# Kernel tuning notes

Hardware: AMD Instinct MI355X
Metric: run time of the kernel (lower is better)

## Reference

```python
import jax, jax.numpy as jnp
import numpy as np

N_NODES = 50000
N_EDGES = 400000
D_PROT = 512
D_TEXT = 2048
GN_EPS = 1e-5


def setup_inputs() -> dict:
    key = jax.random.key(0)
    ks = jax.random.split(key, 8)
    s = 0.02
    return {
        "x": jax.random.normal(ks[0], (N_NODES, D_PROT), jnp.float32),
        "edge_index": jax.random.randint(ks[1], (2, N_EDGES), 0, N_NODES, dtype=jnp.int32),
        "gn_weight": jnp.ones((D_PROT,), jnp.float32),
        "gn_bias": jnp.zeros((D_PROT,), jnp.float32),
        "gn_mean_scale": jnp.ones((D_PROT,), jnp.float32),
        "conv1_w": jax.random.normal(ks[2], (D_PROT, D_PROT), jnp.float32) * s,
        "conv1_b": jnp.zeros((D_PROT,), jnp.float32),
        "conv2_w": jax.random.normal(ks[3], (D_PROT, D_PROT), jnp.float32) * s,
        "conv2_b": jnp.zeros((D_PROT,), jnp.float32),
        "proj1_w": jax.random.normal(ks[4], (D_TEXT, D_PROT), jnp.float32) * s,
        "proj1_b": jnp.zeros((D_TEXT,), jnp.float32),
        "proj2_w": jax.random.normal(ks[5], (D_TEXT, D_TEXT), jnp.float32) * s,
        "proj2_b": jnp.zeros((D_TEXT,), jnp.float32),
    }


def _graph_norm(x, weight, bias, mean_scale):
    # PyG GraphNorm over a single graph: shift by mean_scale*mean, scale by rstd
    mean = jnp.mean(x, axis=0, keepdims=True)            # [1, D]
    out = x - mean * mean_scale
    var = jnp.mean(out * out, axis=0, keepdims=True)     # [1, D]
    out = out * jax.lax.rsqrt(var + GN_EPS)
    return out * weight + bias


def _sgconv(x, src, dst, w, b):
    # SGConv K=1 with GCN normalization and added self-loops:
    n = x.shape[0]
    deg = jax.ops.segment_sum(jnp.ones_like(src, dtype=x.dtype), dst, num_segments=n) + 1.0
    dinv = jax.lax.rsqrt(deg)                            # [N]
    norm = dinv[src] * dinv[dst]                         # [E]
    agg = jax.ops.segment_sum(x[src] * norm[:, None], dst, num_segments=n)
    agg = agg + x * (dinv * dinv)[:, None]               # self-loop contribution
    return agg @ w.T + b


def reference(x, edge_index, gn_weight, gn_bias, gn_mean_scale,
              conv1_w, conv1_b, conv2_w, conv2_b,
              proj1_w, proj1_b, proj2_w, proj2_b):
    src, dst = edge_index[0], edge_index[1]
    h = _graph_norm(x, gn_weight, gn_bias, gn_mean_scale)
    h = jax.nn.relu(_sgconv(h, src, dst, conv1_w, conv1_b))  # dropout = identity (eval)
    h = jax.nn.relu(_sgconv(h, src, dst, conv2_w, conv2_b))
    h = h @ proj1_w.T + proj1_b
    h = jax.nn.gelu(h, approximate=False)
    h = h @ proj2_w.T + proj2_b
    return h
```

## Files before the change

### kernel.cpp

```cpp
#include <hip/hip_runtime.h>
#include <math.h>

typedef _Float16 half_t;
typedef _Float16 f16x2 __attribute__((ext_vector_type(2)));
typedef _Float16 f16x4 __attribute__((ext_vector_type(4)));
typedef _Float16 f16x8 __attribute__((ext_vector_type(8)));
typedef float f32x4 __attribute__((ext_vector_type(4)));

#define D_PROT 512
#define D_TEXT 2048

__global__ void k_cvt4(const float* __restrict__ s, half_t* __restrict__ d, int n4) {
    int i = blockIdx.x * 256 + threadIdx.x;
    if (i < n4) {
        float4 v = ((const float4*)s)[i];
        f16x4 o;
        o.x = (_Float16)v.x; o.y = (_Float16)v.y;
        o.z = (_Float16)v.z; o.w = (_Float16)v.w;
        ((f16x4*)d)[i] = o;
    }
}

__global__ void k_deg(const int* __restrict__ dst, int E, int* __restrict__ deg) {
    int i = blockIdx.x * 256 + threadIdx.x;
    if (i < E) atomicAdd(&deg[dst[i]], 1);
}

__global__ void k_dinv(const int* __restrict__ deg, float* __restrict__ dinv, int n) {
    int i = blockIdx.x * 256 + threadIdx.x;
    if (i < n) dinv[i] = rsqrtf((float)deg[i] + 1.0f);
}

__global__ void k_blocksum(const int* __restrict__ deg, int* __restrict__ bsum, int n) {
    __shared__ int sd[256];
    int i = blockIdx.x * 256 + threadIdx.x;
    sd[threadIdx.x] = (i < n) ? deg[i] : 0;
    __syncthreads();
    for (int s = 128; s > 0; s >>= 1) {
        if (threadIdx.x < s) sd[threadIdx.x] += sd[threadIdx.x + s];
        __syncthreads();
    }
    if (threadIdx.x == 0) bsum[blockIdx.x] = sd[0];
}

__global__ void k_scan_bsum(const int* __restrict__ bsum, int* __restrict__ boff, int nb) {
    if (threadIdx.x == 0 && blockIdx.x == 0) {
        int acc = 0;
        for (int i = 0; i < nb; i++) { boff[i] = acc; acc += bsum[i]; }
    }
}

__global__ void k_scan_final(const int* __restrict__ deg, const int* __restrict__ boff,
                             int* __restrict__ rowptr, int n) {
    __shared__ int sd[256];
    int i = blockIdx.x * 256 + threadIdx.x;
    int v = (i < n) ? deg[i] : 0;
    sd[threadIdx.x] = v;
    __syncthreads();
    for (int s = 1; s < 256; s <<= 1) {
        int t2 = (threadIdx.x >= s) ? sd[threadIdx.x - s] : 0;
        __syncthreads();
        sd[threadIdx.x] += t2;
        __syncthreads();
    }
    if (i < n) rowptr[i + 1] = boff[blockIdx.x] + sd[threadIdx.x];
}

__global__ void k_fill(const int* __restrict__ src, const int* __restrict__ dst, int E,
                       const int* __restrict__ rowptr, int* __restrict__ fill,
                       int* __restrict__ colidx) {
    int i = blockIdx.x * 256 + threadIdx.x;
    if (i < E) {
        int d = dst[i];
        int pos = atomicAdd(&fill[d], 1);
        colidx[rowptr[d] + pos] = src[i];
    }
}

__global__ void k_gnreduce(const float* __restrict__ x, float* __restrict__ sums,
                           float* __restrict__ sumsq, int Nn) {
    int t = threadIdx.x;
    int c = t * 2;
    float s0 = 0, s1 = 0, q0 = 0, q1 = 0;
    for (int r = blockIdx.x; r < Nn; r += gridDim.x) {
        float2 v = *(const float2*)(x + (size_t)r * D_PROT + c);
        s0 += v.x; s1 += v.y; q0 += v.x * v.x; q1 += v.y * v.y;
    }
    atomicAdd(&sums[c], s0);  atomicAdd(&sums[c + 1], s1);
    atomicAdd(&sumsq[c], q0); atomicAdd(&sumsq[c + 1], q1);
}

__global__ void k_gnfinal(const float* __restrict__ sums, const float* __restrict__ sumsq,
                          const float* __restrict__ w, const float* __restrict__ b,
                          const float* __restrict__ ms, float* __restrict__ ab, float invN) {
    int d = blockIdx.x * 256 + threadIdx.x;
    if (d < D_PROT) {
        float mean = sums[d] * invN;
        float m2 = sumsq[d] * invN;
        float mm = mean * ms[d];
        float var = m2 - 2.f * mm * mean + mm * mm;
        float rstd = rsqrtf(var + 1e-5f);
        float a = rstd * w[d];
        ab[d] = a;
        ab[D_PROT + d] = b[d] - mm * a;
    }
}

__global__ void k_gnnorm(const float* __restrict__ x, const float* __restrict__ ab,
                         half_t* __restrict__ h, int n4) {
    int i = blockIdx.x * 256 + threadIdx.x;
    if (i < n4) {
        size_t idx = (size_t)i * 4;
        float4 v = *(const float4*)(x + idx);
        int d = (int)(idx & (D_PROT - 1));
        const float* a = ab;
        const float* bb = ab + D_PROT;
        f16x4 o;
        o.x = (_Float16)(v.x * a[d]     + bb[d]);
        o.y = (_Float16)(v.y * a[d + 1] + bb[d + 1]);
        o.z = (_Float16)(v.z * a[d + 2] + bb[d + 2]);
        o.w = (_Float16)(v.w * a[d + 3] + bb[d + 3]);
        *(f16x4*)(h + idx) = o;
    }
}

__global__ void k_agg(const half_t* __restrict__ h, half_t* __restrict__ out,
                      const int* __restrict__ rowptr, const int* __restrict__ colidx,
                      const float* __restrict__ dinv) {
    int node = blockIdx.x;
    int t = threadIdx.x;
    float di = dinv[node];
    int beg = rowptr[node], end = rowptr[node + 1];
    const f16x4* hp = (const f16x4*)h;
    f16x4 sv = hp[node * 128 + t];
    float dii = di * di;
    float a0 = (float)sv.x * dii, a1 = (float)sv.y * dii;
    float a2 = (float)sv.z * dii, a3 = (float)sv.w * dii;
    int e = beg;
    for (; e + 4 <= end; e += 4) {
        int s0 = colidx[e],     s1 = colidx[e + 1];
        int s2 = colidx[e + 2], s3 = colidx[e + 3];
        float w0 = dinv[s0] * di, w1 = dinv[s1] * di;
        float w2 = dinv[s2] * di, w3 = dinv[s3] * di;
        f16x4 v0 = hp[s0 * 128 + t], v1 = hp[s1 * 128 + t];
        f16x4 v2 = hp[s2 * 128 + t], v3 = hp[s3 * 128 + t];
        a0 += w0 * (float)v0.x + w1 * (float)v1.x + w2 * (float)v2.x + w3 * (float)v3.x;
        a1 += w0 * (float)v0.y + w1 * (float)v1.y + w2 * (float)v2.y + w3 * (float)v3.y;
        a2 += w0 * (float)v0.z + w1 * (float)v1.z + w2 * (float)v2.z + w3 * (float)v3.z;
        a3 += w0 * (float)v0.w + w1 * (float)v1.w + w2 * (float)v2.w + w3 * (float)v3.w;
    }
    for (; e < end; ++e) {
        int s = colidx[e];
        float wgt = dinv[s] * di;
        f16x4 v = hp[s * 128 + t];
        a0 += wgt * (float)v.x; a1 += wgt * (float)v.y;
        a2 += wgt * (float)v.z; a3 += wgt * (float)v.w;
    }
    f16x4 o;
    o.x = (_Float16)a0; o.y = (_Float16)a1; o.z = (_Float16)a2; o.w = (_Float16)a3;
    ((f16x4*)out)[node * 128 + t] = o;
}

#define FENCE() asm volatile("" ::: "memory")
#define BAR()   do { FENCE(); __builtin_amdgcn_s_barrier(); FENCE(); } while (0)
#define WAITV4() asm volatile("s_waitcnt vmcnt(4)" ::: "memory")
#define WAITV0() asm volatile("s_waitcnt vmcnt(0)" ::: "memory")
#define GLD(src, dst) __builtin_amdgcn_global_load_lds( \
    (const __attribute__((address_space(1))) void*)(src), \
    (__attribute__((address_space(3))) void*)(dst), 16, 0, 0)
#define LDF(base, row, kk) \
    (*(const f16x8*)((base) + ((((row) * 128 + (kk) * 64 + fqo)) ^ (((row) & 7) << 4))))
#define MM(mi, nj, A_, B_) \
    acc[mi][nj] = __builtin_amdgcn_mfma_f32_16x16x32_f16(A_, B_, acc[mi][nj], 0, 0, 0)

template <int ACT, typename OUT_T>
__global__ __launch_bounds__(512, 2) void k_gemm8(const half_t* __restrict__ A,
                                                  const half_t* __restrict__ W,
                                                  const float* __restrict__ bias,
                                                  OUT_T* __restrict__ C,
                                                  int M, int N, int K) {
    __shared__ half_t sm[2][32768];
    const int bn = blockIdx.x * 256;
    const int bm = blockIdx.y * 256;

    const int t = threadIdx.x;
    const int w = t >> 6, lane = t & 63;
    const int fr = lane & 15, fq = lane >> 4;
    const int fqo = fq * 16;
    const int wm = (w >> 2) * 128, wn = (w & 3) * 64;
    const int NT = K >> 6;

    int q0 = w * 512 + lane * 8;
    int q1 = 4096 + q0;
    int s0 = q0 ^ (((q0 >> 6) & 7) << 3);
    int s1 = q1 ^ (((q1 >> 6) & 7) << 3);
    int r0 = s0 >> 6, c0 = s0 & 63;
    int r1 = s1 >> 6, c1 = s1 & 63;
    const half_t* gAlo0 = A + (size_t)min(bm + r0, M - 1) * K + c0;
    const half_t* gAlo1 = A + (size_t)min(bm + r1, M - 1) * K + c1;
    const half_t* gAhi0 = A + (size_t)min(bm + 128 + r0, M - 1) * K + c0;
    const half_t* gAhi1 = A + (size_t)min(bm + 128 + r1, M - 1) * K + c1;
    const half_t* gBlo0 = W + (size_t)(bn + r0) * K + c0;
    const half_t* gBlo1 = W + (size_t)(bn + r1) * K + c1;
    const half_t* gBhi0 = W + (size_t)(bn + 128 + r0) * K + c0;
    const half_t* gBhi1 = W + (size_t)(bn + 128 + r1) * K + c1;
    const int dst0 = w * 512;

#define STAGE_ALO(buf, kt) do {                                                \
    GLD(gAlo0 + (size_t)(kt) * 64, &sm[buf][dst0]);                            \
    GLD(gAlo1 + (size_t)(kt) * 64, &sm[buf][4096 + dst0]);                     \
} while (0)
#define STAGE_AHI(buf, kt) do {                                                \
    GLD(gAhi0 + (size_t)(kt) * 64, &sm[buf][8192 + dst0]);                     \
    GLD(gAhi1 + (size_t)(kt) * 64, &sm[buf][12288 + dst0]);                    \
} while (0)
#define STAGE_BLO(buf, kt) do {                                                \
    GLD(gBlo0 + (size_t)(kt) * 64, &sm[buf][16384 + dst0]);                    \
    GLD(gBlo1 + (size_t)(kt) * 64, &sm[buf][20480 + dst0]);                    \
} while (0)
#define STAGE_BHI(buf, kt) do {                                                \
    GLD(gBhi0 + (size_t)(kt) * 64, &sm[buf][24576 + dst0]);                    \
    GLD(gBhi1 + (size_t)(kt) * 64, &sm[buf][28672 + dst0]);                    \
} while (0)

    f32x4 acc[8][4] = {};

    STAGE_ALO(0, 0); STAGE_AHI(0, 0); STAGE_BLO(0, 0); STAGE_BHI(0, 0);
    {
        int k1 = (NT > 1) ? 1 : 0;
        STAGE_BLO(1, k1); STAGE_BHI(1, k1);
    }
    WAITV4();
    BAR();

#define TILE(cur, nxt, tt) do {                                                 \
    const char* smA = (const char*)&sm[cur][0];                                 \
    const char* smB = (const char*)&sm[cur][16384];                             \
    const int kA = ((tt) + 1 < NT) ? (tt) + 1 : NT - 1;                         \
    const int kB = ((tt) + 2 < NT) ? (tt) + 2 : NT - 1;                         \
                        \
    f16x8 b00 = LDF(smB, wn + fr, 0),      b01 = LDF(smB, wn + fr, 1);          \
    f16x8 b10 = LDF(smB, wn + 16 + fr, 0), b11 = LDF(smB, wn + 16 + fr, 1);     \
    f16x8 b20 = LDF(smB, wn + 32 + fr, 0), b21 = LDF(smB, wn + 32 + fr, 1);     \
    f16x8 b30 = LDF(smB, wn + 48 + fr, 0), b31 = LDF(smB, wn + 48 + fr, 1);     \
    f16x8 a00 = LDF(smA, wm + fr, 0),      a01 = LDF(smA, wm + fr, 1);          \
    f16x8 a10 = LDF(smA, wm + 16 + fr, 0), a11 = LDF(smA, wm + 16 + fr, 1);     \
    STAGE_ALO(nxt, kA);                                                         \
    BAR();                                                                      \
    __builtin_amdgcn_s_setprio(1);                                              \
    MM(0, 0, a00, b00); MM(0, 1, a00, b10); MM(0, 2, a00, b20); MM(0, 3, a00, b30); \
    MM(0, 0, a01, b01); MM(0, 1, a01, b11); MM(0, 2, a01, b21); MM(0, 3, a01, b31); \
    MM(1, 0, a10, b00); MM(1, 1, a10, b10); MM(1, 2, a10, b20); MM(1, 3, a10, b30); \
    MM(1, 0, a11, b01); MM(1, 1, a11, b11); MM(1, 2, a11, b21); MM(1, 3, a11, b31); \
    __builtin_amdgcn_s_setprio(0);                                              \
    BAR();                                                                      \
                                \
    f16x8 a20 = LDF(smA, wm + 32 + fr, 0), a21 = LDF(smA, wm + 32 + fr, 1);     \
    f16x8 a30 = LDF(smA, wm + 48 + fr, 0), a31 = LDF(smA, wm + 48 + fr, 1);     \
    STAGE_AHI(nxt, kA);                                                         \
    BAR();                                                                      \
    __builtin_amdgcn_s_setprio(1);                                              \
    MM(2, 0, a20, b00); MM(2, 1, a20, b10); MM(2, 2, a20, b20); MM(2, 3, a20, b30); \
    MM(2, 0, a21, b01); MM(2, 1, a21, b11); MM(2, 2, a21, b21); MM(2, 3, a21, b31); \
    MM(3, 0, a30, b00); MM(3, 1, a30, b10); MM(3, 2, a30, b20); MM(3, 3, a30, b30); \
    MM(3, 0, a31, b01); MM(3, 1, a31, b11); MM(3, 2, a31, b21); MM(3, 3, a31, b31); \
    __builtin_amdgcn_s_setprio(0);                                              \
    BAR();                                                                      \
                                \
    f16x8 a40 = LDF(smA, wm + 64 + fr, 0), a41 = LDF(smA, wm + 64 + fr, 1);     \
    f16x8 a50 = LDF(smA, wm + 80 + fr, 0), a51 = LDF(smA, wm + 80 + fr, 1);     \
    STAGE_BLO(cur, kB);                                                         \
    BAR();                                                                      \
    __builtin_amdgcn_s_setprio(1);                                              \
    MM(4, 0, a40, b00); MM(4, 1, a40, b10); MM(4, 2, a40, b20); MM(4, 3, a40, b30); \
    MM(4, 0, a41, b01); MM(4, 1, a41, b11); MM(4, 2, a41, b21); MM(4, 3, a41, b31); \
    MM(5, 0, a50, b00); MM(5, 1, a50, b10); MM(5, 2, a50, b20); MM(5, 3, a50, b30); \
    MM(5, 0, a51, b01); MM(5, 1, a51, b11); MM(5, 2, a51, b21); MM(5, 3, a51, b31); \
    __builtin_amdgcn_s_setprio(0);                                              \
    BAR();                                                                      \
                  \
    f16x8 a60 = LDF(smA, wm + 96 + fr, 0),  a61 = LDF(smA, wm + 96 + fr, 1);    \
    f16x8 a70 = LDF(smA, wm + 112 + fr, 0), a71 = LDF(smA, wm + 112 + fr, 1);   \
    STAGE_BHI(cur, kB);                                                         \
    BAR();                                                                      \
    __builtin_amdgcn_s_setprio(1);                                              \
    MM(6, 0, a60, b00); MM(6, 1, a60, b10); MM(6, 2, a60, b20); MM(6, 3, a60, b30); \
    MM(6, 0, a61, b01); MM(6, 1, a61, b11); MM(6, 2, a61, b21); MM(6, 3, a61, b31); \
    MM(7, 0, a70, b00); MM(7, 1, a70, b10); MM(7, 2, a70, b20); MM(7, 3, a70, b30); \
    MM(7, 0, a71, b01); MM(7, 1, a71, b11); MM(7, 2, a71, b21); MM(7, 3, a71, b31); \
    __builtin_amdgcn_s_setprio(0);                                              \
    WAITV4();                                                                   \
    BAR();                                                                      \
} while (0)

    for (int tt = 0; tt < NT; tt += 2) {
        TILE(0, 1, tt);
        TILE(1, 0, tt + 1);
    }
    WAITV0();
#undef TILE
#undef STAGE_ALO
#undef STAGE_AHI
#undef STAGE_BLO
#undef STAGE_BHI

    const int col0 = bn + wn + fr;
#pragma unroll
    for (int mi = 0; mi < 8; mi++) {
        int rb = bm + wm + mi * 16 + fq * 4;
#pragma unroll
        for (int nj = 0; nj < 4; nj++) {
            int col = col0 + nj * 16;
            float bv = bias[col];
#pragma unroll
            for (int r = 0; r < 4; r++) {
                int row = rb + r;
                if (row < M) {
                    float v = acc[mi][nj][r] + bv;
                    if (ACT == 1) v = fmaxf(v, 0.f);
                    if (ACT == 2) v = 0.5f * v * (1.f + erff(v * 0.70710678118f));
                    C[(size_t)row * N + col] = (OUT_T)v;
                }
            }
        }
    }
}

extern "C" void kernel_launch(void* const* d_in, const int* in_sizes, int n_in,
                              void* d_out, int out_size, void* d_ws, size_t ws_size,
                              hipStream_t stream) {
    const float* x     = (const float*)d_in[0];
    const int*   eidx  = (const int*)d_in[1];
    const float* gn_w  = (const float*)d_in[2];
    const float* gn_b  = (const float*)d_in[3];
    const float* gn_ms = (const float*)d_in[4];
    const float* w1    = (const float*)d_in[5];
    const float* b1    = (const float*)d_in[6];
    const float* w2    = (const float*)d_in[7];
    const float* b2    = (const float*)d_in[8];
    const float* p1    = (const float*)d_in[9];
    const float* pb1   = (const float*)d_in[10];
    const float* p2    = (const float*)d_in[11];
    const float* pb2   = (const float*)d_in[12];

    const int Nn = in_sizes[0] / D_PROT;
    const int E  = in_sizes[1] / 2;
    const int M  = Nn;

    char* ws = (char*)d_ws;
    size_t off = 0;
    auto alloc = [&](size_t bytes) {
        void* p = ws + off;
        off += (bytes + 255) & ~(size_t)255;
        return p;
    };
    half_t* w1h    = (half_t*)alloc((size_t)D_PROT * D_PROT * 2);
    half_t* w2h    = (half_t*)alloc((size_t)D_PROT * D_PROT * 2);
    half_t* p1h    = (half_t*)alloc((size_t)D_TEXT * D_PROT * 2);
    half_t* p2h    = (half_t*)alloc((size_t)D_TEXT * D_TEXT * 2);
    int*    deg    = (int*)alloc((size_t)Nn * 4);
    float*  dinv   = (float*)alloc((size_t)Nn * 4);
    int*    rowptr = (int*)alloc((size_t)(Nn + 1) * 4);
    int*    fillc  = (int*)alloc((size_t)Nn * 4);
    int*    bsum   = (int*)alloc(1024);
    int*    boff   = (int*)alloc(1024);
    int*    colidx = (int*)alloc((size_t)E * 4);
    float*  sums   = (float*)alloc(D_PROT * 4);
    float*  sumsq  = (float*)alloc(D_PROT * 4);
    float*  gnab   = (float*)alloc(2 * D_PROT * 4);
    half_t* buf1   = (half_t*)alloc((size_t)Nn * D_PROT * 2);
    half_t* buf2   = (half_t*)alloc((size_t)Nn * D_PROT * 2);
    half_t* big    = (half_t*)alloc((size_t)Nn * D_TEXT * 2);

    const int* esrc = eidx;
    const int* edst = eidx + E;

    hipMemsetAsync(deg, 0, (size_t)Nn * 4, stream);
    hipMemsetAsync(fillc, 0, (size_t)Nn * 4, stream);
    hipMemsetAsync(rowptr, 0, (size_t)(Nn + 1) * 4, stream);
    hipMemsetAsync(sums, 0, D_PROT * 4, stream);
    hipMemsetAsync(sumsq, 0, D_PROT * 4, stream);

    k_cvt4<<<(D_PROT * D_PROT / 4 + 255) / 256, 256, 0, stream>>>(w1, w1h, D_PROT * D_PROT / 4);
    k_cvt4<<<(D_PROT * D_PROT / 4 + 255) / 256, 256, 0, stream>>>(w2, w2h, D_PROT * D_PROT / 4);
    k_cvt4<<<(D_TEXT * D_PROT / 4 + 255) / 256, 256, 0, stream>>>(p1, p1h, D_TEXT * D_PROT / 4);
    k_cvt4<<<(D_TEXT * D_TEXT / 4 + 255) / 256, 256, 0, stream>>>(p2, p2h, D_TEXT * D_TEXT / 4);

    int eb = (E + 255) / 256;
    int nb = (Nn + 255) / 256;
    k_deg<<<eb, 256, 0, stream>>>(edst, E, deg);
    k_dinv<<<nb, 256, 0, stream>>>(deg, dinv, Nn);
    k_blocksum<<<nb, 256, 0, stream>>>(deg, bsum, Nn);
    k_scan_bsum<<<1, 1, 0, stream>>>(bsum, boff, nb);
    k_scan_final<<<nb, 256, 0, stream>>>(deg, boff, rowptr, Nn);
    k_fill<<<eb, 256, 0, stream>>>(esrc, edst, E, rowptr, fillc, colidx);

    k_gnreduce<<<256, 256, 0, stream>>>(x, sums, sumsq, Nn);
    k_gnfinal<<<2, 256, 0, stream>>>(sums, sumsq, gn_w, gn_b, gn_ms, gnab, 1.0f / (float)Nn);
    int n4 = Nn * D_PROT / 4;
    k_gnnorm<<<(n4 + 255) / 256, 256, 0, stream>>>(x, gnab, buf1, n4);

    const int mt256 = (M + 255) / 256;

    k_agg<<<Nn, 128, 0, stream>>>(buf1, buf2, rowptr, colidx, dinv);
    {
        dim3 g(D_PROT / 256, mt256);
        k_gemm8<1, half_t><<<g, 512, 0, stream>>>(buf2, w1h, b1, buf1, M, D_PROT, D_PROT);
    }
    k_agg<<<Nn, 128, 0, stream>>>(buf1, buf2, rowptr, colidx, dinv);
    {
        dim3 g(D_PROT / 256, mt256);
        k_gemm8<1, half_t><<<g, 512, 0, stream>>>(buf2, w2h, b2, buf1, M, D_PROT, D_PROT);
    }
    {
        dim3 g(D_TEXT / 256, mt256);
        k_gemm8<2, half_t><<<g, 512, 0, stream>>>(buf1, p1h, pb1, big, M, D_TEXT, D_PROT);
    }
    {
        dim3 g(D_TEXT / 256, mt256);
        k_gemm8<0, float><<<g, 512, 0, stream>>>(big, p2h, pb2, (float*)d_out, M, D_TEXT, D_TEXT);
    }
}
```

Measured before the change: 1.253 ms.

## Restructure GEMM main loop to two phases and remap workgroups across XCDs

The GEMM tile loop goes from four barrier-separated sub-phases to two. All A and B fragments are loaded from LDS up front, with an explicit lgkmcnt wait before the mid barrier, and the global-to-LDS staging of the next tiles is issued in two larger groups. Workgroup IDs are also remapped round-robin across the 8 XCDs so neighbouring tiles share an L2. This cuts barrier count and is meant to improve cache locality, at the cost of higher register pressure from holding all 16 A fragments at once, which risks spills or lower occupancy.

```diff
diff --git a/kernel.cpp b/kernel.cpp
--- a/kernel.cpp
+++ b/kernel.cpp
@@ -165,6 +165,7 @@
 #define BAR()   do { FENCE(); __builtin_amdgcn_s_barrier(); FENCE(); } while (0)
 #define WAITV4() asm volatile("s_waitcnt vmcnt(4)" ::: "memory")
 #define WAITV0() asm volatile("s_waitcnt vmcnt(0)" ::: "memory")
+#define LGKM0()  asm volatile("s_waitcnt lgkmcnt(0)" ::: "memory")
 #define GLD(src, dst) __builtin_amdgcn_global_load_lds( \
     (const __attribute__((address_space(1))) void*)(src), \
     (__attribute__((address_space(3))) void*)(dst), 16, 0, 0)
@@ -180,8 +181,12 @@
                                                   OUT_T* __restrict__ C,
                                                   int M, int N, int K) {
     __shared__ half_t sm[2][32768];
-    const int bn = blockIdx.x * 256;
-    const int bm = blockIdx.y * 256;
+    const int gx = gridDim.x;
+    const int nwg = gx * gridDim.y;
+    int b = blockIdx.y * gx + blockIdx.x;
+    int w8 = ((nwg & 7) == 0) ? (b & 7) * (nwg >> 3) + (b >> 3) : b;
+    const int bn = (w8 % gx) * 256;
+    const int bm = (w8 / gx) * 256;
 
     const int t = threadIdx.x;
     const int w = t >> 6, lane = t & 63;
@@ -206,30 +211,23 @@
     const half_t* gBhi1 = W + (size_t)(bn + 128 + r1) * K + c1;
     const int dst0 = w * 512;
 
-#define STAGE_ALO(buf, kt) do {                                                \
+#define STAGE_A(buf, kt) do {                                                  \
     GLD(gAlo0 + (size_t)(kt) * 64, &sm[buf][dst0]);                            \
     GLD(gAlo1 + (size_t)(kt) * 64, &sm[buf][4096 + dst0]);                     \
-} while (0)
-#define STAGE_AHI(buf, kt) do {                                                \
     GLD(gAhi0 + (size_t)(kt) * 64, &sm[buf][8192 + dst0]);                     \
     GLD(gAhi1 + (size_t)(kt) * 64, &sm[buf][12288 + dst0]);                    \
 } while (0)
-#define STAGE_BLO(buf, kt) do {                                                \
+#define STAGE_B(buf, kt) do {                                                  \
     GLD(gBlo0 + (size_t)(kt) * 64, &sm[buf][16384 + dst0]);                    \
     GLD(gBlo1 + (size_t)(kt) * 64, &sm[buf][20480 + dst0]);                    \
-} while (0)
-#define STAGE_BHI(buf, kt) do {                                                \
     GLD(gBhi0 + (size_t)(kt) * 64, &sm[buf][24576 + dst0]);                    \
     GLD(gBhi1 + (size_t)(kt) * 64, &sm[buf][28672 + dst0]);                    \
 } while (0)
 
     f32x4 acc[8][4] = {};
 
-    STAGE_ALO(0, 0); STAGE_AHI(0, 0); STAGE_BLO(0, 0); STAGE_BHI(0, 0);
-    {
-        int k1 = (NT > 1) ? 1 : 0;
-        STAGE_BLO(1, k1); STAGE_BHI(1, k1);
-    }
+    STAGE_A(0, 0); STAGE_B(0, 0);
+    STAGE_B(1, (NT > 1) ? 1 : 0);
     WAITV4();
     BAR();
 
@@ -238,58 +236,40 @@
     const char* smB = (const char*)&sm[cur][16384];                             \
     const int kA = ((tt) + 1 < NT) ? (tt) + 1 : NT - 1;                         \
     const int kB = ((tt) + 2 < NT) ? (tt) + 2 : NT - 1;                         \
-                        \
-    f16x8 b00 = LDF(smB, wn + fr, 0),      b01 = LDF(smB, wn + fr, 1);          \
-    f16x8 b10 = LDF(smB, wn + 16 + fr, 0), b11 = LDF(smB, wn + 16 + fr, 1);     \
-    f16x8 b20 = LDF(smB, wn + 32 + fr, 0), b21 = LDF(smB, wn + 32 + fr, 1);     \
-    f16x8 b30 = LDF(smB, wn + 48 + fr, 0), b31 = LDF(smB, wn + 48 + fr, 1);     \
-    f16x8 a00 = LDF(smA, wm + fr, 0),      a01 = LDF(smA, wm + fr, 1);          \
-    f16x8 a10 = LDF(smA, wm + 16 + fr, 0), a11 = LDF(smA, wm + 16 + fr, 1);     \
-    STAGE_ALO(nxt, kA);                                                         \
-    BAR();                                                                      \
+    STAGE_A(nxt, kA);          \
+    f16x8 bf[4][2], af[8][2];                                                   \
+    _Pragma("unroll")                                                           \
+    for (int nj = 0; nj < 4; nj++) {                                            \
+        bf[nj][0] = LDF(smB, wn + nj * 16 + fr, 0);                             \
+        bf[nj][1] = LDF(smB, wn + nj * 16 + fr, 1);                             \
+    }                                                                           \
+    _Pragma("unroll")                                                           \
+    for (int mi = 0; mi < 8; mi++) {                                            \
+        af[mi][0] = LDF(smA, wm + mi * 16 + fr, 0);                             \
+        af[mi][1] = LDF(smA, wm + mi * 16 + fr, 1);                             \
+    }                                                                           \
     __builtin_amdgcn_s_setprio(1);                                              \
-    MM(0, 0, a00, b00); MM(0, 1, a00, b10); MM(0, 2, a00, b20); MM(0, 3, a00, b30); \
-    MM(0, 0, a01, b01); MM(0, 1, a01, b11); MM(0, 2, a01, b21); MM(0, 3, a01, b31); \
-    MM(1, 0, a10, b00); MM(1, 1, a10, b10); MM(1, 2, a10, b20); MM(1, 3, a10, b30); \
-    MM(1, 0, a11, b01); MM(1, 1, a11, b11); MM(1, 2, a11, b21); MM(1, 3, a11, b31); \
+    _Pragma("unroll")                                                           \
+    for (int mi = 0; mi < 4; mi++)                                              \
+        _Pragma("unroll")                                                       \
+        for (int nj = 0; nj < 4; nj++) {                                        \
+            MM(mi, nj, af[mi][0], bf[nj][0]);                                   \
+            MM(mi, nj, af[mi][1], bf[nj][1]);                                   \
+        }                                                                       \
     __builtin_amdgcn_s_setprio(0);                                              \
-    BAR();                                                                      \
-                                \
-    f16x8 a20 = LDF(smA, wm + 32 + fr, 0), a21 = LDF(smA, wm + 32 + fr, 1);     \
-    f16x8 a30 = LDF(smA, wm + 48 + fr, 0), a31 = LDF(smA, wm + 48 + fr, 1);     \
-    STAGE_AHI(nxt, kA);                                                         \
-    BAR();                                                                      \
+    LGKM0();                           \
+    BAR();                                \
+    STAGE_B(cur, kB);                                                           \
     __builtin_amdgcn_s_setprio(1);                                              \
-    MM(2, 0, a20, b00); MM(2, 1, a20, b10); MM(2, 2, a20, b20); MM(2, 3, a20, b30); \
-    MM(2, 0, a21, b01); MM(2, 1, a21, b11); MM(2, 2, a21, b21); MM(2, 3, a21, b31); \
-    MM(3, 0, a30, b00); MM(3, 1, a30, b10); MM(3, 2, a30, b20); MM(3, 3, a30, b30); \
-    MM(3, 0, a31, b01); MM(3, 1, a31, b11); MM(3, 2, a31, b21); MM(3, 3, a31, b31); \
+    _Pragma("unroll")                                                           \
+    for (int mi = 4; mi < 8; mi++)                                              \
+        _Pragma("unroll")                                                       \
+        for (int nj = 0; nj < 4; nj++) {                                        \
+            MM(mi, nj, af[mi][0], bf[nj][0]);                                   \
+            MM(mi, nj, af[mi][1], bf[nj][1]);                                   \
+        }                                                                       \
     __builtin_amdgcn_s_setprio(0);                                              \
-    BAR();                                                                      \
-                                \
-    f16x8 a40 = LDF(smA, wm + 64 + fr, 0), a41 = LDF(smA, wm + 64 + fr, 1);     \
-    f16x8 a50 = LDF(smA, wm + 80 + fr, 0), a51 = LDF(smA, wm + 80 + fr, 1);     \
-    STAGE_BLO(cur, kB);                                                         \
-    BAR();                                                                      \
-    __builtin_amdgcn_s_setprio(1);                                              \
-    MM(4, 0, a40, b00); MM(4, 1, a40, b10); MM(4, 2, a40, b20); MM(4, 3, a40, b30); \
-    MM(4, 0, a41, b01); MM(4, 1, a41, b11); MM(4, 2, a41, b21); MM(4, 3, a41, b31); \
-    MM(5, 0, a50, b00); MM(5, 1, a50, b10); MM(5, 2, a50, b20); MM(5, 3, a50, b30); \
-    MM(5, 0, a51, b01); MM(5, 1, a51, b11); MM(5, 2, a51, b21); MM(5, 3, a51, b31); \
-    __builtin_amdgcn_s_setprio(0);                                              \
-    BAR();                                                                      \
-                  \
-    f16x8 a60 = LDF(smA, wm + 96 + fr, 0),  a61 = LDF(smA, wm + 96 + fr, 1);    \
-    f16x8 a70 = LDF(smA, wm + 112 + fr, 0), a71 = LDF(smA, wm + 112 + fr, 1);   \
-    STAGE_BHI(cur, kB);                                                         \
-    BAR();                                                                      \
-    __builtin_amdgcn_s_setprio(1);                                              \
-    MM(6, 0, a60, b00); MM(6, 1, a60, b10); MM(6, 2, a60, b20); MM(6, 3, a60, b30); \
-    MM(6, 0, a61, b01); MM(6, 1, a61, b11); MM(6, 2, a61, b21); MM(6, 3, a61, b31); \
-    MM(7, 0, a70, b00); MM(7, 1, a70, b10); MM(7, 2, a70, b20); MM(7, 3, a70, b30); \
-    MM(7, 0, a71, b01); MM(7, 1, a71, b11); MM(7, 2, a71, b21); MM(7, 3, a71, b31); \
-    __builtin_amdgcn_s_setprio(0);                                              \
-    WAITV4();                                                                   \
+    WAITV4();             \
     BAR();                                                                      \
 } while (0)
 
@@ -299,10 +279,8 @@
     }
     WAITV0();
 #undef TILE
-#undef STAGE_ALO
-#undef STAGE_AHI
-#undef STAGE_BLO
-#undef STAGE_BHI
+#undef STAGE_A
+#undef STAGE_B
 
     const int col0 = bn + wn + fr;
 #pragma unroll
```

Measured after the change: 2.015 ms. 60.9% more time.
